# Performance work log

Measured on AMD Instinct MI355X. Metric: run time of the kernel, lower is better.

## Reference

```python
import jax, jax.numpy as jnp
import numpy as np

EMBED_DIM = 768
NUM_HEADS = 12
HEAD_DIM = EMBED_DIM // NUM_HEADS
ROPE_BASE = 10000.0


def setup_inputs() -> dict:
    key = jax.random.key(0)
    k1, k2, k3, k4, k5 = jax.random.split(key, 5)
    B, S, E = 1, 4096, EMBED_DIM
    x = jax.random.normal(k1, (B, S, E), dtype=jnp.float32)
    # causal mask: 1 where attend allowed, 0 elsewhere
    mask = jnp.tril(jnp.ones((S, S), dtype=jnp.int32))
    scale = 1.0 / np.sqrt(E)
    Wqkv = jax.random.normal(k2, (E, 3 * E), dtype=jnp.float32) * scale
    bqkv = jax.random.normal(k3, (3 * E,), dtype=jnp.float32) * 0.01
    Wout = jax.random.normal(k4, (E, E), dtype=jnp.float32) * scale
    bout = jax.random.normal(k5, (E,), dtype=jnp.float32) * 0.01
    return {"x": x, "mask": mask, "Wqkv": Wqkv, "bqkv": bqkv, "Wout": Wout, "bout": bout}


def _rope_cos_sin(seq_len, dtype):
    inv_freq = 1.0 / (ROPE_BASE ** (jnp.arange(0, HEAD_DIM, 2, dtype=jnp.float32) / HEAD_DIM))
    t = jnp.arange(seq_len, dtype=dtype)
    freqs = jnp.outer(t, inv_freq.astype(dtype))  # [S, Dh/2]
    emb = jnp.concatenate([freqs, freqs], axis=-1)  # [S, Dh]
    return jnp.cos(emb), jnp.sin(emb)


def _rotate_half(u):
    u1, u2 = jnp.split(u, 2, axis=-1)
    return jnp.concatenate([-u2, u1], axis=-1)


def reference(x, mask, Wqkv, bqkv, Wout, bout):
    B, S, E = x.shape
    H, Dh = NUM_HEADS, HEAD_DIM
    qkv = x @ Wqkv + bqkv  # [B, S, 3E]
    qkv = qkv.reshape(B, S, 3, H, Dh).transpose(2, 0, 3, 1, 4)  # [3, B, H, S, Dh]
    Q, K, V = qkv[0], qkv[1], qkv[2]
    # RoPE
    cos, sin = _rope_cos_sin(S, x.dtype)  # [S, Dh]
    cos = cos[None, None]
    sin = sin[None, None]
    Q = Q * cos + _rotate_half(Q) * sin
    K = K * cos + _rotate_half(K) * sin
    scores = jnp.einsum('bhsd,bhtd->bhst', Q, K) / jnp.sqrt(jnp.asarray(Dh, x.dtype))
    scores = jnp.where(mask[None, None] == 0, jnp.finfo(x.dtype).min, scores)
    attn = jax.nn.softmax(scores, axis=-1)  # dropout p=0 (eval) -> identity
    out = jnp.einsum('bhst,bhtd->bhsd', attn, V)  # [B, H, S, Dh]
    out = out.transpose(0, 2, 1, 3).reshape(B, S, E)
    return out @ Wout + bout
```

## Files before the change

kernel.cpp:

```cpp
#include <hip/hip_runtime.h>

typedef unsigned short u16;
typedef unsigned int   u32;
using short8 = __attribute__((ext_vector_type(8))) short;
using f32x4  = __attribute__((ext_vector_type(4))) float;
using f32x16 = __attribute__((ext_vector_type(16))) float;
using u32x4  = __attribute__((ext_vector_type(4))) unsigned int;

#define S_LEN 4096
#define EMB   768
#define NH    12
#define DH    64

#define QSCALE 0.18033688011112042f

__device__ __forceinline__ u16 f2bf(float f) {
  unsigned int u = __builtin_bit_cast(unsigned int, f);
  u += 0x7fffu + ((u >> 16) & 1u);
  return (u16)(u >> 16);
}

__device__ __forceinline__ u32 cvtpk(float lo, float hi) {
  u32 r;
  asm("v_cvt_pk_bf16_f32 %0, %1, %2" : "=v"(r) : "v"(lo), "v"(hi));
  return r;
}

__device__ __forceinline__ float pr_max(float v) {
  return fmaxf(v, __shfl_xor(v, 32));
}
__device__ __forceinline__ float pr_add(float v) {
  return v + __shfl_xor(v, 32);
}

__device__ __forceinline__ float fexp2(float x) {
#if __has_builtin(__builtin_amdgcn_exp2f)
  return __builtin_amdgcn_exp2f(x);
#else
  return exp2f(x);
#endif
}

__device__ __forceinline__ f32x4 mfma16(short8 a, short8 b, f32x4 c) {
  return __builtin_amdgcn_mfma_f32_16x16x32_bf16(a, b, c, 0, 0, 0);
}
__device__ __forceinline__ f32x16 mfma32(short8 a, short8 b, f32x16 c) {
  return __builtin_amdgcn_mfma_f32_32x32x16_bf16(a, b, c, 0, 0, 0);
}

__device__ __forceinline__ short8 pack_frag(u32 w0, u32 w1, u32 w2, u32 w3, bool hi) {
  u32 x0 = (u32)__shfl_xor((int)w0, 32), x1 = (u32)__shfl_xor((int)w1, 32);
  u32 x2 = (u32)__shfl_xor((int)w2, 32), x3 = (u32)__shfl_xor((int)w3, 32);
  u32x4 f = { hi ? x2 : w0, hi ? x3 : w1, hi ? w2 : x0, hi ? w3 : x1 };
  return __builtin_bit_cast(short8, f);
}


__global__ void k_conv_x(const float* __restrict__ x, u16* __restrict__ xb, int n) {
  int i = blockIdx.x * 256 + threadIdx.x;
  if (i < n) xb[i] = f2bf(x[i]);
}

__global__ __launch_bounds__(256) void k_transpose_w(const float* __restrict__ w,
                                                     u16* __restrict__ wt,
                                                     int rows, int cols) {
  __shared__ float tile[32][33];
  int tx = threadIdx.x & 31, ty = threadIdx.x >> 5;
  int kb = blockIdx.x * 32;
  int nb = blockIdx.y * 32;
#pragma unroll
  for (int j = 0; j < 4; j++)
    tile[ty + 8 * j][tx] = w[(size_t)(kb + ty + 8 * j) * cols + nb + tx];
  __syncthreads();
#pragma unroll
  for (int j = 0; j < 4; j++)
    wt[(size_t)(nb + ty + 8 * j) * rows + kb + tx] = f2bf(tile[tx][ty + 8 * j]);
}

__global__ __launch_bounds__(256) void k_qkv(const u16* __restrict__ A,
                                             const u16* __restrict__ Bt,
                                             const float* __restrict__ bias,
                                             u16* __restrict__ Qb,
                                             u16* __restrict__ Kb,
                                             u16* __restrict__ Vt) {
  __shared__ u16 As[128][40];
  __shared__ u16 Bs[128][40];
  int t = threadIdx.x;
  int w = t >> 6, lane = t & 63, g = lane >> 4, c = lane & 15;
  int wr = w >> 1, wc = w & 1;
  int bm = blockIdx.x * 128, bn = blockIdx.y * 128;

  f32x4 acc[4][4];
#pragma unroll
  for (int m = 0; m < 4; m++)
#pragma unroll
    for (int n = 0; n < 4; n++) acc[m][n] = (f32x4){0.f, 0.f, 0.f, 0.f};

  int srow = t >> 1, sseg = (t & 1) * 16;
  for (int bk = 0; bk < EMB; bk += 32) {
    const u16* ga = A  + (size_t)(bm + srow) * EMB + bk + sseg;
    const u16* gb = Bt + (size_t)(bn + srow) * EMB + bk + sseg;
    short8 a0 = *(const short8*)ga, a1 = *(const short8*)(ga + 8);
    short8 b0 = *(const short8*)gb, b1 = *(const short8*)(gb + 8);
    __syncthreads();
    *(short8*)&As[srow][sseg] = a0; *(short8*)&As[srow][sseg + 8] = a1;
    *(short8*)&Bs[srow][sseg] = b0; *(short8*)&Bs[srow][sseg + 8] = b1;
    __syncthreads();
    short8 af[4], bf[4];
#pragma unroll
    for (int m = 0; m < 4; m++) af[m] = *(const short8*)&As[wr * 64 + m * 16 + c][g * 8];
#pragma unroll
    for (int n = 0; n < 4; n++) bf[n] = *(const short8*)&Bs[wc * 64 + n * 16 + c][g * 8];
#pragma unroll
    for (int m = 0; m < 4; m++)
#pragma unroll
      for (int n = 0; n < 4; n++) acc[m][n] = mfma16(af[m], bf[n], acc[m][n]);
  }

  int colbase = bn + wc * 64;
  int sec = colbase / EMB;
  int hh  = (colbase % EMB) / DH;
  float qs = (sec == 0) ? QSCALE : 1.0f;
  float invf[2];
#pragma unroll
  for (int n = 0; n < 2; n++) {
    int d1 = n * 16 + c;
    invf[n] = exp2f(-(float)d1 * (13.287712379549449f / 32.0f));
  }
#pragma unroll
  for (int m = 0; m < 4; m++) {
    int rowb = bm + wr * 64 + m * 16 + 4 * g;
#pragma unroll
    for (int e = 0; e < 4; e++) {
      int srw = rowb + e;
      float v[4];
#pragma unroll
      for (int n = 0; n < 4; n++) v[n] = acc[m][n][e] + bias[colbase + n * 16 + c];
      if (sec == 2) {
#pragma unroll
        for (int n = 0; n < 4; n++)
          Vt[(size_t)(hh * DH + n * 16 + c) * S_LEN + srw] = f2bf(v[n]);
      } else {
        u16* dst = (sec == 0) ? Qb : Kb;
        size_t base = ((size_t)hh * S_LEN + srw) * DH;
#pragma unroll
        for (int n = 0; n < 2; n++) {
          int d1 = n * 16 + c;
          float ang = (float)srw * invf[n];
          float sn, cs;
          sincosf(ang, &sn, &cs);
          float o1 = (v[n] * cs - v[n + 2] * sn) * qs;
          float o2 = (v[n + 2] * cs + v[n] * sn) * qs;
          dst[base + d1]      = f2bf(o1);
          dst[base + d1 + 32] = f2bf(o2);
        }
      }
    }
  }
}


template<bool MASKED>
__device__ __forceinline__ void attn_tile(int kv0, int qi, int half,
    const u16* __restrict__ Kh, const u16* __restrict__ Vh,
    short8 qf0, short8 qf1, short8 qf2, short8 qf3,
    f32x16& acc0, f32x16& acc1, float& m, float& l) {
  const u16* kp = Kh + (size_t)(kv0 + qi) * DH + half * 8;
  short8 k0 = *(const short8*)(kp);
  short8 k1 = *(const short8*)(kp + 16);
  short8 k2 = *(const short8*)(kp + 32);
  short8 k3 = *(const short8*)(kp + 48);
  __builtin_amdgcn_s_setprio(1);
  f32x16 sc = {0,0,0,0,0,0,0,0,0,0,0,0,0,0,0,0};
  sc = mfma32(k0, qf0, sc);
  sc = mfma32(k1, qf1, sc);
  sc = mfma32(k2, qf2, sc);
  sc = mfma32(k3, qf3, sc);
  __builtin_amdgcn_s_setprio(0);
  const u16* vp = Vh + (size_t)qi * S_LEN + kv0 + half * 8;
  short8 v00 = *(const short8*)(vp);
  short8 v01 = *(const short8*)(vp + 16);
  short8 v10 = *(const short8*)(vp + (size_t)32 * S_LEN);
  short8 v11 = *(const short8*)(vp + (size_t)32 * S_LEN + 16);
  if (MASKED) {
#pragma unroll
    for (int i = 0; i < 16; i++) {
      int kl = (i & 3) + 8 * (i >> 2) + 4 * half;
      if (kl > qi) sc[i] = -1e30f;
    }
  }
  float t0 = fmaxf(fmaxf(sc[0], sc[1]), fmaxf(sc[2], sc[3]));
  float t1 = fmaxf(fmaxf(sc[4], sc[5]), fmaxf(sc[6], sc[7]));
  float t2 = fmaxf(fmaxf(sc[8], sc[9]), fmaxf(sc[10], sc[11]));
  float t3 = fmaxf(fmaxf(sc[12], sc[13]), fmaxf(sc[14], sc[15]));
  float rmax = pr_max(fmaxf(fmaxf(t0, t1), fmaxf(t2, t3)));
  if (__any(rmax > m + 8.0f)) {
    float mn = fmaxf(m, rmax);
    float f = fexp2(m - mn);
    m = mn; l *= f;
#pragma unroll
    for (int i = 0; i < 16; i++) { acc0[i] *= f; acc1[i] *= f; }
  }
  f32x16 p;
#pragma unroll
  for (int i = 0; i < 16; i++) p[i] = fexp2(sc[i] - m);
  l += ((p[0] + p[1]) + (p[2] + p[3])) + ((p[4] + p[5]) + (p[6] + p[7]))
     + ((p[8] + p[9]) + (p[10] + p[11])) + ((p[12] + p[13]) + (p[14] + p[15]));
  bool hi = (half != 0);
  short8 pa0 = pack_frag(cvtpk(p[0], p[1]),   cvtpk(p[2], p[3]),
                         cvtpk(p[4], p[5]),   cvtpk(p[6], p[7]), hi);
  short8 pa1 = pack_frag(cvtpk(p[8], p[9]),   cvtpk(p[10], p[11]),
                         cvtpk(p[12], p[13]), cvtpk(p[14], p[15]), hi);
  __builtin_amdgcn_s_setprio(1);
  acc0 = mfma32(v00, pa0, acc0);
  acc0 = mfma32(v01, pa1, acc0);
  acc1 = mfma32(v10, pa0, acc1);
  acc1 = mfma32(v11, pa1, acc1);
  __builtin_amdgcn_s_setprio(0);
}

__device__ __forceinline__ void attn_tile2(int kv0, int qi, int half,
    const u16* __restrict__ Kh, const u16* __restrict__ Vh,
    short8 qf0, short8 qf1, short8 qf2, short8 qf3,
    f32x16& acc0, f32x16& acc1, float& m, float& l) {
  const u16* kpa = Kh + (size_t)(kv0 + qi) * DH + half * 8;
  const u16* kpb = kpa + (size_t)32 * DH;
  short8 ka0 = *(const short8*)(kpa);
  short8 ka1 = *(const short8*)(kpa + 16);
  short8 ka2 = *(const short8*)(kpa + 32);
  short8 ka3 = *(const short8*)(kpa + 48);
  short8 kb0 = *(const short8*)(kpb);
  short8 kb1 = *(const short8*)(kpb + 16);
  short8 kb2 = *(const short8*)(kpb + 32);
  short8 kb3 = *(const short8*)(kpb + 48);
  __builtin_amdgcn_s_setprio(1);
  f32x16 sa = {0,0,0,0,0,0,0,0,0,0,0,0,0,0,0,0};
  f32x16 sb = {0,0,0,0,0,0,0,0,0,0,0,0,0,0,0,0};
  sa = mfma32(ka0, qf0, sa);
  sb = mfma32(kb0, qf0, sb);
  sa = mfma32(ka1, qf1, sa);
  sb = mfma32(kb1, qf1, sb);
  sa = mfma32(ka2, qf2, sa);
  sb = mfma32(kb2, qf2, sb);
  sa = mfma32(ka3, qf3, sa);
  sb = mfma32(kb3, qf3, sb);
  __builtin_amdgcn_s_setprio(0);
  const u16* vpa = Vh + (size_t)qi * S_LEN + kv0 + half * 8;
  const u16* vpb = vpa + 32;
  short8 va00 = *(const short8*)(vpa);
  short8 va01 = *(const short8*)(vpa + 16);
  short8 va10 = *(const short8*)(vpa + (size_t)32 * S_LEN);
  short8 va11 = *(const short8*)(vpa + (size_t)32 * S_LEN + 16);
  short8 vb00 = *(const short8*)(vpb);
  short8 vb01 = *(const short8*)(vpb + 16);
  short8 vb10 = *(const short8*)(vpb + (size_t)32 * S_LEN);
  short8 vb11 = *(const short8*)(vpb + (size_t)32 * S_LEN + 16);
  float t0 = fmaxf(fmaxf(sa[0], sa[1]), fmaxf(sa[2], sa[3]));
  float t1 = fmaxf(fmaxf(sa[4], sa[5]), fmaxf(sa[6], sa[7]));
  float t2 = fmaxf(fmaxf(sa[8], sa[9]), fmaxf(sa[10], sa[11]));
  float t3 = fmaxf(fmaxf(sa[12], sa[13]), fmaxf(sa[14], sa[15]));
  float u0 = fmaxf(fmaxf(sb[0], sb[1]), fmaxf(sb[2], sb[3]));
  float u1 = fmaxf(fmaxf(sb[4], sb[5]), fmaxf(sb[6], sb[7]));
  float u2 = fmaxf(fmaxf(sb[8], sb[9]), fmaxf(sb[10], sb[11]));
  float u3 = fmaxf(fmaxf(sb[12], sb[13]), fmaxf(sb[14], sb[15]));
  float rmax = pr_max(fmaxf(fmaxf(fmaxf(t0, t1), fmaxf(t2, t3)),
                            fmaxf(fmaxf(u0, u1), fmaxf(u2, u3))));
  if (__any(rmax > m + 8.0f)) {
    float mn = fmaxf(m, rmax);
    float f = fexp2(m - mn);
    m = mn; l *= f;
#pragma unroll
    for (int i = 0; i < 16; i++) { acc0[i] *= f; acc1[i] *= f; }
  }
  f32x16 pa, pb;
#pragma unroll
  for (int i = 0; i < 16; i++) pa[i] = fexp2(sa[i] - m);
#pragma unroll
  for (int i = 0; i < 16; i++) pb[i] = fexp2(sb[i] - m);
  float la = ((pa[0] + pa[1]) + (pa[2] + pa[3])) + ((pa[4] + pa[5]) + (pa[6] + pa[7]))
           + ((pa[8] + pa[9]) + (pa[10] + pa[11])) + ((pa[12] + pa[13]) + (pa[14] + pa[15]));
  float lb = ((pb[0] + pb[1]) + (pb[2] + pb[3])) + ((pb[4] + pb[5]) + (pb[6] + pb[7]))
           + ((pb[8] + pb[9]) + (pb[10] + pb[11])) + ((pb[12] + pb[13]) + (pb[14] + pb[15]));
  l += la + lb;
  bool hi = (half != 0);
  short8 fa0 = pack_frag(cvtpk(pa[0], pa[1]),   cvtpk(pa[2], pa[3]),
                         cvtpk(pa[4], pa[5]),   cvtpk(pa[6], pa[7]), hi);
  short8 fa1 = pack_frag(cvtpk(pa[8], pa[9]),   cvtpk(pa[10], pa[11]),
                         cvtpk(pa[12], pa[13]), cvtpk(pa[14], pa[15]), hi);
  short8 fb0 = pack_frag(cvtpk(pb[0], pb[1]),   cvtpk(pb[2], pb[3]),
                         cvtpk(pb[4], pb[5]),   cvtpk(pb[6], pb[7]), hi);
  short8 fb1 = pack_frag(cvtpk(pb[8], pb[9]),   cvtpk(pb[10], pb[11]),
                         cvtpk(pb[12], pb[13]), cvtpk(pb[14], pb[15]), hi);
  __builtin_amdgcn_s_setprio(1);
  acc0 = mfma32(va00, fa0, acc0);
  acc1 = mfma32(va10, fa0, acc1);
  acc0 = mfma32(va01, fa1, acc0);
  acc1 = mfma32(va11, fa1, acc1);
  acc0 = mfma32(vb00, fb0, acc0);
  acc1 = mfma32(vb10, fb0, acc1);
  acc0 = mfma32(vb01, fb1, acc0);
  acc1 = mfma32(vb11, fb1, acc1);
  __builtin_amdgcn_s_setprio(0);
}

__global__ __launch_bounds__(256, 3) void k_attn(const u16* __restrict__ Q,
                                                 const u16* __restrict__ K,
                                                 const u16* __restrict__ Vt,
                                                 u16* __restrict__ O) {
  __shared__ float Lacc[3][64][33];
  __shared__ float Lml[2][3][32];

  int t = threadIdx.x;
  int w = t >> 6, lane = t & 63;
  int qi = lane & 31, half = lane >> 5;
  int b = blockIdx.x;
  int h = b % NH;
  int qb = 127 - b / NH;

  const u16* Qh = Q  + (size_t)h * S_LEN * DH;
  const u16* Kh = K  + (size_t)h * S_LEN * DH;
  const u16* Vh = Vt + (size_t)h * DH * S_LEN;

  const u16* qp = Qh + (size_t)(qb * 32 + qi) * DH + half * 8;
  short8 qf0 = *(const short8*)(qp);
  short8 qf1 = *(const short8*)(qp + 16);
  short8 qf2 = *(const short8*)(qp + 32);
  short8 qf3 = *(const short8*)(qp + 48);

  f32x16 acc0 = {0,0,0,0,0,0,0,0,0,0,0,0,0,0,0,0};
  f32x16 acc1 = {0,0,0,0,0,0,0,0,0,0,0,0,0,0,0,0};
  float m = -1e30f, l = 0.f;

  int nt = qb + 1;
  int ck = (nt + 3) >> 2;
  int start = w * ck;
  int end   = min(start + ck, nt);
  int endu  = min(end, nt - 1);
  int tt = start;
#pragma unroll 1
  for (; tt + 1 < endu; tt += 2)
    attn_tile2(tt * 32, qi, half, Kh, Vh, qf0, qf1, qf2, qf3, acc0, acc1, m, l);
  for (; tt < endu; tt++)
    attn_tile<false>(tt * 32, qi, half, Kh, Vh, qf0, qf1, qf2, qf3, acc0, acc1, m, l);
  if (start < nt && end == nt)
    attn_tile<true>((nt - 1) * 32, qi, half, Kh, Vh, qf0, qf1, qf2, qf3, acc0, acc1, m, l);

  float l2 = pr_add(l);
  if (w > 0) {
#pragma unroll
    for (int i = 0; i < 16; i++) {
      Lacc[w - 1][lane][i]      = acc0[i];
      Lacc[w - 1][lane][16 + i] = acc1[i];
    }
    if (half == 0) { Lml[0][w - 1][qi] = m; Lml[1][w - 1][qi] = l2; }
  }
  __syncthreads();
  if (w == 0) {
    float mw[3], lw[3];
    float M = m;
#pragma unroll
    for (int j = 0; j < 3; j++) { mw[j] = Lml[0][j][qi]; lw[j] = Lml[1][j][qi]; M = fmaxf(M, mw[j]); }
    float f0 = fexp2(m - M);
    float ltot = l2 * f0;
#pragma unroll
    for (int i = 0; i < 16; i++) { acc0[i] *= f0; acc1[i] *= f0; }
#pragma unroll
    for (int j = 0; j < 3; j++) {
      float fj = fexp2(mw[j] - M);
      ltot += lw[j] * fj;
#pragma unroll
      for (int i = 0; i < 16; i++) {
        acc0[i] += fj * Lacc[j][lane][i];
        acc1[i] += fj * Lacc[j][lane][16 + i];
      }
    }
    float rl = 1.0f / ltot;
    u16* orow = O + (size_t)(qb * 32 + qi) * EMB + h * DH;
#pragma unroll
    for (int i = 0; i < 16; i += 2) {
      int dl = (i & 3) + 8 * (i >> 2) + 4 * half;
      u32 wa = cvtpk(acc0[i] * rl, acc0[i + 1] * rl);
      u32 wb = cvtpk(acc1[i] * rl, acc1[i + 1] * rl);
      *(u32*)(orow + dl)      = wa;
      *(u32*)(orow + 32 + dl) = wb;
    }
  }
}

__global__ __launch_bounds__(256) void k_out(const u16* __restrict__ A,
                                             const u16* __restrict__ Bt,
                                             const float* __restrict__ bias,
                                             float* __restrict__ out) {
  __shared__ u16 As[128][40];
  __shared__ u16 Bs[128][40];
  int t = threadIdx.x;
  int w = t >> 6, lane = t & 63, g = lane >> 4, c = lane & 15;
  int wr = w >> 1, wc = w & 1;
  int bm = blockIdx.x * 128, bn = blockIdx.y * 128;

  f32x4 acc[4][4];
#pragma unroll
  for (int m = 0; m < 4; m++)
#pragma unroll
    for (int n = 0; n < 4; n++) acc[m][n] = (f32x4){0.f, 0.f, 0.f, 0.f};

  int srow = t >> 1, sseg = (t & 1) * 16;
  for (int bk = 0; bk < EMB; bk += 32) {
    const u16* ga = A  + (size_t)(bm + srow) * EMB + bk + sseg;
    const u16* gb = Bt + (size_t)(bn + srow) * EMB + bk + sseg;
    short8 a0 = *(const short8*)ga, a1 = *(const short8*)(ga + 8);
    short8 b0 = *(const short8*)gb, b1 = *(const short8*)(gb + 8);
    __syncthreads();
    *(short8*)&As[srow][sseg] = a0; *(short8*)&As[srow][sseg + 8] = a1;
    *(short8*)&Bs[srow][sseg] = b0; *(short8*)&Bs[srow][sseg + 8] = b1;
    __syncthreads();
    short8 af[4], bf[4];
#pragma unroll
    for (int m = 0; m < 4; m++) af[m] = *(const short8*)&As[wr * 64 + m * 16 + c][g * 8];
#pragma unroll
    for (int n = 0; n < 4; n++) bf[n] = *(const short8*)&Bs[wc * 64 + n * 16 + c][g * 8];
#pragma unroll
    for (int m = 0; m < 4; m++)
#pragma unroll
      for (int n = 0; n < 4; n++) acc[m][n] = mfma16(af[m], bf[n], acc[m][n]);
  }
  int colbase = bn + wc * 64;
#pragma unroll
  for (int m = 0; m < 4; m++) {
    int rowb = bm + wr * 64 + m * 16 + 4 * g;
#pragma unroll
    for (int e = 0; e < 4; e++) {
      int srw = rowb + e;
#pragma unroll
      for (int n = 0; n < 4; n++) {
        int col = colbase + n * 16 + c;
        out[(size_t)srw * EMB + col] = acc[m][n][e] + bias[col];
      }
    }
  }
}


extern "C" void kernel_launch(void* const* d_in, const int* in_sizes, int n_in,
                              void* d_out, int out_size, void* d_ws, size_t ws_size,
                              hipStream_t stream) {
  const float* x    = (const float*)d_in[0];
  const float* Wqkv = (const float*)d_in[2];
  const float* bqkv = (const float*)d_in[3];
  const float* Wout = (const float*)d_in[4];
  const float* bout = (const float*)d_in[5];
  float* out = (float*)d_out;

  char* ws = (char*)d_ws;
  u16* xb     = (u16*)(ws);
  u16* wqkvt  = (u16*)(ws + 6291456);
  u16* woutt  = (u16*)(ws + 9830400);
  u16* Qb     = (u16*)(ws + 11010048);
  u16* Kb     = (u16*)(ws + 17301504);
  u16* Vtb    = (u16*)(ws + 23592960);
  u16* Ob     = (u16*)(ws + 29884416);

  k_conv_x<<<(S_LEN * EMB + 255) / 256, 256, 0, stream>>>(x, xb, S_LEN * EMB);
  k_transpose_w<<<dim3(EMB / 32, 3 * EMB / 32), 256, 0, stream>>>(Wqkv, wqkvt, EMB, 3 * EMB);
  k_transpose_w<<<dim3(EMB / 32, EMB / 32), 256, 0, stream>>>(Wout, woutt, EMB, EMB);

  k_qkv<<<dim3(32, 18), 256, 0, stream>>>(xb, wqkvt, bqkv, Qb, Kb, Vtb);
  k_attn<<<NH * 128, 256, 0, stream>>>(Qb, Kb, Vtb, Ob);
  k_out<<<dim3(32, 6), 256, 0, stream>>>(Ob, woutt, bout, out);
}
```

Baseline: 178.2 us.

## Fuse x bf16 conversion into QKV GEMM and halve out-proj tile width

Drops the separate x-to-bf16 conversion kernel and has the QKV GEMM load fp32 x directly, converting to bf16 with packed conversion instructions while staging into shared memory. This removes one launch and a full write plus re-read of the bf16 copy of x, but each QKV block now reads fp32 x (twice the bytes) and repeats the conversion across all 18 column blocks. The output projection tile also shrinks from 128x128 to 128x64, doubling the grid from 192 to 384 blocks to fill more compute units, at the cost of less data reuse per block.

```diff
diff --git a/kernel.cpp b/kernel.cpp
--- a/kernel.cpp
+++ b/kernel.cpp
@@ -26,6 +26,14 @@
   return r;
 }
 
+__device__ __forceinline__ short8 pack8(const float* p) {
+  f32x4 x0 = *(const f32x4*)p;
+  f32x4 x1 = *(const f32x4*)(p + 4);
+  u32x4 r = { cvtpk(x0[0], x0[1]), cvtpk(x0[2], x0[3]),
+              cvtpk(x1[0], x1[1]), cvtpk(x1[2], x1[3]) };
+  return __builtin_bit_cast(short8, r);
+}
+
 __device__ __forceinline__ float pr_max(float v) {
   return fmaxf(v, __shfl_xor(v, 32));
 }
@@ -55,11 +63,6 @@
   return __builtin_bit_cast(short8, f);
 }
 
-
-__global__ void k_conv_x(const float* __restrict__ x, u16* __restrict__ xb, int n) {
-  int i = blockIdx.x * 256 + threadIdx.x;
-  if (i < n) xb[i] = f2bf(x[i]);
-}
 
 __global__ __launch_bounds__(256) void k_transpose_w(const float* __restrict__ w,
                                                      u16* __restrict__ wt,
@@ -77,7 +80,7 @@
     wt[(size_t)(nb + ty + 8 * j) * rows + kb + tx] = f2bf(tile[tx][ty + 8 * j]);
 }
 
-__global__ __launch_bounds__(256) void k_qkv(const u16* __restrict__ A,
+__global__ __launch_bounds__(256) void k_qkv(const float* __restrict__ X,
                                              const u16* __restrict__ Bt,
                                              const float* __restrict__ bias,
                                              u16* __restrict__ Qb,
@@ -98,9 +101,10 @@
 
   int srow = t >> 1, sseg = (t & 1) * 16;
   for (int bk = 0; bk < EMB; bk += 32) {
-    const u16* ga = A  + (size_t)(bm + srow) * EMB + bk + sseg;
-    const u16* gb = Bt + (size_t)(bn + srow) * EMB + bk + sseg;
-    short8 a0 = *(const short8*)ga, a1 = *(const short8*)(ga + 8);
+    const float* gx = X + (size_t)(bm + srow) * EMB + bk + sseg;
+    const u16*   gb = Bt + (size_t)(bn + srow) * EMB + bk + sseg;
+    short8 a0 = pack8(gx);
+    short8 a1 = pack8(gx + 8);
     short8 b0 = *(const short8*)gb, b1 = *(const short8*)(gb + 8);
     __syncthreads();
     *(short8*)&As[srow][sseg] = a0; *(short8*)&As[srow][sseg + 8] = a1;
@@ -392,48 +396,47 @@
                                              const float* __restrict__ bias,
                                              float* __restrict__ out) {
   __shared__ u16 As[128][40];
-  __shared__ u16 Bs[128][40];
+  __shared__ u16 Bs[64][40];
   int t = threadIdx.x;
   int w = t >> 6, lane = t & 63, g = lane >> 4, c = lane & 15;
-  int wr = w >> 1, wc = w & 1;
-  int bm = blockIdx.x * 128, bn = blockIdx.y * 128;
-
-  f32x4 acc[4][4];
-#pragma unroll
-  for (int m = 0; m < 4; m++)
+  int bm = blockIdx.x * 128, bn = blockIdx.y * 64;
+
+  f32x4 acc[2][4];
+#pragma unroll
+  for (int m = 0; m < 2; m++)
 #pragma unroll
     for (int n = 0; n < 4; n++) acc[m][n] = (f32x4){0.f, 0.f, 0.f, 0.f};
 
-  int srow = t >> 1, sseg = (t & 1) * 16;
+  int arow = t >> 1, aseg = (t & 1) * 16;
+  int brow = t >> 2, bseg = (t & 3) * 8;
   for (int bk = 0; bk < EMB; bk += 32) {
-    const u16* ga = A  + (size_t)(bm + srow) * EMB + bk + sseg;
-    const u16* gb = Bt + (size_t)(bn + srow) * EMB + bk + sseg;
+    const u16* ga = A  + (size_t)(bm + arow) * EMB + bk + aseg;
+    const u16* gb = Bt + (size_t)(bn + brow) * EMB + bk + bseg;
     short8 a0 = *(const short8*)ga, a1 = *(const short8*)(ga + 8);
-    short8 b0 = *(const short8*)gb, b1 = *(const short8*)(gb + 8);
+    short8 b0 = *(const short8*)gb;
     __syncthreads();
-    *(short8*)&As[srow][sseg] = a0; *(short8*)&As[srow][sseg + 8] = a1;
-    *(short8*)&Bs[srow][sseg] = b0; *(short8*)&Bs[srow][sseg + 8] = b1;
+    *(short8*)&As[arow][aseg] = a0; *(short8*)&As[arow][aseg + 8] = a1;
+    *(short8*)&Bs[brow][bseg] = b0;
     __syncthreads();
-    short8 af[4], bf[4];
-#pragma unroll
-    for (int m = 0; m < 4; m++) af[m] = *(const short8*)&As[wr * 64 + m * 16 + c][g * 8];
-#pragma unroll
-    for (int n = 0; n < 4; n++) bf[n] = *(const short8*)&Bs[wc * 64 + n * 16 + c][g * 8];
-#pragma unroll
-    for (int m = 0; m < 4; m++)
+    short8 af[2], bf[4];
+#pragma unroll
+    for (int m = 0; m < 2; m++) af[m] = *(const short8*)&As[w * 32 + m * 16 + c][g * 8];
+#pragma unroll
+    for (int n = 0; n < 4; n++) bf[n] = *(const short8*)&Bs[n * 16 + c][g * 8];
+#pragma unroll
+    for (int m = 0; m < 2; m++)
 #pragma unroll
       for (int n = 0; n < 4; n++) acc[m][n] = mfma16(af[m], bf[n], acc[m][n]);
   }
-  int colbase = bn + wc * 64;
-#pragma unroll
-  for (int m = 0; m < 4; m++) {
-    int rowb = bm + wr * 64 + m * 16 + 4 * g;
+#pragma unroll
+  for (int m = 0; m < 2; m++) {
+    int rowb = bm + w * 32 + m * 16 + 4 * g;
 #pragma unroll
     for (int e = 0; e < 4; e++) {
       int srw = rowb + e;
 #pragma unroll
       for (int n = 0; n < 4; n++) {
-        int col = colbase + n * 16 + c;
+        int col = bn + n * 16 + c;
         out[(size_t)srw * EMB + col] = acc[m][n][e] + bias[col];
       }
     }
@@ -452,7 +455,6 @@
   float* out = (float*)d_out;
 
   char* ws = (char*)d_ws;
-  u16* xb     = (u16*)(ws);
   u16* wqkvt  = (u16*)(ws + 6291456);
   u16* woutt  = (u16*)(ws + 9830400);
   u16* Qb     = (u16*)(ws + 11010048);
@@ -460,11 +462,10 @@
   u16* Vtb    = (u16*)(ws + 23592960);
   u16* Ob     = (u16*)(ws + 29884416);
 
-  k_conv_x<<<(S_LEN * EMB + 255) / 256, 256, 0, stream>>>(x, xb, S_LEN * EMB);
   k_transpose_w<<<dim3(EMB / 32, 3 * EMB / 32), 256, 0, stream>>>(Wqkv, wqkvt, EMB, 3 * EMB);
   k_transpose_w<<<dim3(EMB / 32, EMB / 32), 256, 0, stream>>>(Wout, woutt, EMB, EMB);
 
-  k_qkv<<<dim3(32, 18), 256, 0, stream>>>(xb, wqkvt, bqkv, Qb, Kb, Vtb);
+  k_qkv<<<dim3(32, 18), 256, 0, stream>>>(x, wqkvt, bqkv, Qb, Kb, Vtb);
   k_attn<<<NH * 128, 256, 0, stream>>>(Qb, Kb, Vtb, Ob);
-  k_out<<<dim3(32, 6), 256, 0, stream>>>(Ob, woutt, bout, out);
-}
+  k_out<<<dim3(32, 12), 256, 0, stream>>>(Ob, woutt, bout, out);
+}
```

Result: slower. 183.4 us (+2.9%).
